# Optimization experiments

Measured on AMD Instinct MI355X. Metric: run time of the kernel, lower is better.

The kernel has to match this reference:

```python
import jax, jax.numpy as jnp
import numpy as np

N_NODES = 50000


def setup_inputs() -> dict:
    key = jax.random.key(0)
    k1, k2, k3, k4, k5, k6 = jax.random.split(key, 6)
    feature = jax.random.normal(k1, (N_NODES, 128), dtype=jnp.float32)
    norm = jax.random.uniform(k2, (N_NODES, 1), dtype=jnp.float32)
    W = jax.random.normal(k3, (128, 128), dtype=jnp.float32) * 0.05
    b = jax.random.normal(k4, (128,), dtype=jnp.float32) * 0.05
    src = jax.random.randint(k5, (600000,), 0, N_NODES, dtype=jnp.int32)
    dst = jax.random.randint(k6, (600000,), 0, N_NODES, dtype=jnp.int32)
    return {"feature": feature, "norm": norm, "W": W, "b": b, "src": src, "dst": dst}


def reference(feature, norm, W, b, src, dst):
    n = feature.shape[0]
    # message: h_src * norm_src, gathered per edge  [E, d]
    msg = feature[src] * norm[src]
    # scatter-sum into destination nodes, then scale by norm_dst
    accum = jax.ops.segment_sum(msg, dst, num_segments=n) * norm
    # DGL semantics: nodes with zero in-degree keep their original feature
    in_deg = jax.ops.segment_sum(jnp.ones((dst.shape[0],), dtype=jnp.float32), dst, num_segments=n)
    h = jnp.where(in_deg[:, None] > 0, accum, feature)
    # node apply: linear + relu
    return jax.nn.relu(h @ W.T + b)
```

## Files before the change

kernel.cpp:

```cpp
#include <hip/hip_runtime.h>

#define N_NODES 50000
#define N_EDGES 600000
#define D 128
#define CAP 64

typedef __attribute__((ext_vector_type(8))) short bf16x8;
typedef __attribute__((ext_vector_type(4))) float f32x4;
typedef __attribute__((ext_vector_type(4))) unsigned short ushort4v;

__device__ inline unsigned int f2bf_u(float f) {
    unsigned int u = __builtin_bit_cast(unsigned int, f);
    return (u + 0x7FFFu + ((u >> 16) & 1u)) >> 16;
}
__device__ inline unsigned int pack2(float lo, float hi) {
    return f2bf_u(lo) | (f2bf_u(hi) << 16);
}
__device__ inline float bf_lo(unsigned int u) {
    return __builtin_bit_cast(float, u << 16);
}
__device__ inline float bf_hi(unsigned int u) {
    return __builtin_bit_cast(float, u & 0xFFFF0000u);
}

__global__ __launch_bounds__(256) void setup_kernel(
    const float* __restrict__ W, unsigned short* __restrict__ Wb,
    int* __restrict__ cursor)
{
    const int b = blockIdx.x, t = threadIdx.x;
    if (b < 16) {
        int j = b * 256 + t;
        float4 w = *reinterpret_cast<const float4*>(W + (size_t)j * 4);
        ushort4 o;
        o.x = (unsigned short)f2bf_u(w.x);
        o.y = (unsigned short)f2bf_u(w.y);
        o.z = (unsigned short)f2bf_u(w.z);
        o.w = (unsigned short)f2bf_u(w.w);
        *reinterpret_cast<ushort4*>(Wb + (size_t)j * 4) = o;
    } else {
        int idx = (b - 16) * 256 + t;
        if (idx < 12500) *reinterpret_cast<int4*>(cursor + idx * 4) = make_int4(0, 0, 0, 0);
    }
}

__global__ __launch_bounds__(256) void prefill_kernel(
    const int* __restrict__ src, const int* __restrict__ dst,
    const float* __restrict__ feat, const float* __restrict__ norm,
    int* __restrict__ cursor, unsigned short* __restrict__ csr16,
    unsigned short* __restrict__ g)
{
    const int b = blockIdx.x, t = threadIdx.x;
    if (b < 2344) {
        int e = b * 256 + t;
        if (e < N_EDGES) {
            int d = dst[e];
            int slot = atomicAdd(&cursor[d], 1);
            if (slot < CAP) csr16[((size_t)d << 6) + slot] = (unsigned short)src[e];
        }
    } else {
        int gid = (b - 2344) * 256 + t;
        int row = gid >> 4;
        int c8  = (gid & 15) * 8;
        float nr = norm[row];
        float4 f0 = *reinterpret_cast<const float4*>(feat + (size_t)row * D + c8);
        float4 f1 = *reinterpret_cast<const float4*>(feat + (size_t)row * D + c8 + 4);
        uint4 o;
        o.x = pack2(f0.x * nr, f0.y * nr);
        o.y = pack2(f0.z * nr, f0.w * nr);
        o.z = pack2(f1.x * nr, f1.y * nr);
        o.w = pack2(f1.z * nr, f1.w * nr);
        *reinterpret_cast<uint4*>(g + (size_t)row * D + c8) = o;
    }
}

__global__ __launch_bounds__(256) void gather_mfma(
    const unsigned short* __restrict__ g,
    const float* __restrict__ feat, const float* __restrict__ norm,
    const int* __restrict__ cursor,
    const unsigned short* __restrict__ csr16,
    const unsigned short* __restrict__ Wb,
    const float* __restrict__ bias,
    float* __restrict__ out)
{
    __shared__ __align__(16) unsigned short hsh[16 * 136];
    const int t    = threadIdx.x;
    const int w    = t >> 6;
    const int lane = t & 63;
    const int kg   = lane >> 4;
    const int mr   = lane & 15;
    const int nbase = blockIdx.x * 16;

    const int ln   = w * 4 + kg;
    const int node = nbase + ln;
    const int deg  = min(cursor[node], CAP);
    const int base = node << 6;

    float a0 = 0.f, a1 = 0.f, a2 = 0.f, a3 = 0.f;
    float a4 = 0.f, a5 = 0.f, a6 = 0.f, a7 = 0.f;
    const unsigned short* gcol = g + mr * 8;

    int i = 0;
    for (; i + 4 <= deg; i += 4) {
        ushort4v ix = *reinterpret_cast<const ushort4v*>(csr16 + base + i);
        uint4 v0 = *reinterpret_cast<const uint4*>(gcol + (size_t)ix[0] * D);
        uint4 v1 = *reinterpret_cast<const uint4*>(gcol + (size_t)ix[1] * D);
        uint4 v2 = *reinterpret_cast<const uint4*>(gcol + (size_t)ix[2] * D);
        uint4 v3 = *reinterpret_cast<const uint4*>(gcol + (size_t)ix[3] * D);
        a0 += bf_lo(v0.x) + bf_lo(v1.x) + bf_lo(v2.x) + bf_lo(v3.x);
        a1 += bf_hi(v0.x) + bf_hi(v1.x) + bf_hi(v2.x) + bf_hi(v3.x);
        a2 += bf_lo(v0.y) + bf_lo(v1.y) + bf_lo(v2.y) + bf_lo(v3.y);
        a3 += bf_hi(v0.y) + bf_hi(v1.y) + bf_hi(v2.y) + bf_hi(v3.y);
        a4 += bf_lo(v0.z) + bf_lo(v1.z) + bf_lo(v2.z) + bf_lo(v3.z);
        a5 += bf_hi(v0.z) + bf_hi(v1.z) + bf_hi(v2.z) + bf_hi(v3.z);
        a6 += bf_lo(v0.w) + bf_lo(v1.w) + bf_lo(v2.w) + bf_lo(v3.w);
        a7 += bf_hi(v0.w) + bf_hi(v1.w) + bf_hi(v2.w) + bf_hi(v3.w);
    }
    for (; i < deg; ++i) {
        unsigned short s0 = csr16[base + i];
        uint4 v0 = *reinterpret_cast<const uint4*>(gcol + (size_t)s0 * D);
        a0 += bf_lo(v0.x); a1 += bf_hi(v0.x);
        a2 += bf_lo(v0.y); a3 += bf_hi(v0.y);
        a4 += bf_lo(v0.z); a5 += bf_hi(v0.z);
        a6 += bf_lo(v0.w); a7 += bf_hi(v0.w);
    }

    if (deg == 0) {
        float4 f0 = *reinterpret_cast<const float4*>(feat + (size_t)node * D + mr * 8);
        float4 f1 = *reinterpret_cast<const float4*>(feat + (size_t)node * D + mr * 8 + 4);
        a0 = f0.x; a1 = f0.y; a2 = f0.z; a3 = f0.w;
        a4 = f1.x; a5 = f1.y; a6 = f1.z; a7 = f1.w;
    } else {
        float nd = norm[node];
        a0 *= nd; a1 *= nd; a2 *= nd; a3 *= nd;
        a4 *= nd; a5 *= nd; a6 *= nd; a7 *= nd;
    }
    uint4 o;
    o.x = pack2(a0, a1);
    o.y = pack2(a2, a3);
    o.z = pack2(a4, a5);
    o.w = pack2(a6, a7);
    *reinterpret_cast<uint4*>(&hsh[ln * 136 + mr * 8]) = o;
    __syncthreads();

    bf16x8 fa0 = *reinterpret_cast<const bf16x8*>(&hsh[mr * 136 + kg * 8]);
    bf16x8 fa1 = *reinterpret_cast<const bf16x8*>(&hsh[mr * 136 + kg * 8 + 32]);
    bf16x8 fa2 = *reinterpret_cast<const bf16x8*>(&hsh[mr * 136 + kg * 8 + 64]);
    bf16x8 fa3 = *reinterpret_cast<const bf16x8*>(&hsh[mr * 136 + kg * 8 + 96]);

    const int orow0 = nbase + kg * 4;
    #pragma unroll
    for (int nn = 0; nn < 2; ++nn) {
        const int n0 = w * 2 + nn;
        const size_t bbase = (size_t)(n0 * 16 + mr) * D + kg * 8;
        bf16x8 b0 = *reinterpret_cast<const bf16x8*>(Wb + bbase);
        bf16x8 b1 = *reinterpret_cast<const bf16x8*>(Wb + bbase + 32);
        bf16x8 b2 = *reinterpret_cast<const bf16x8*>(Wb + bbase + 64);
        bf16x8 b3 = *reinterpret_cast<const bf16x8*>(Wb + bbase + 96);
        f32x4 acc = {0.f, 0.f, 0.f, 0.f};
        acc = __builtin_amdgcn_mfma_f32_16x16x32_bf16(fa0, b0, acc, 0, 0, 0);
        acc = __builtin_amdgcn_mfma_f32_16x16x32_bf16(fa1, b1, acc, 0, 0, 0);
        acc = __builtin_amdgcn_mfma_f32_16x16x32_bf16(fa2, b2, acc, 0, 0, 0);
        acc = __builtin_amdgcn_mfma_f32_16x16x32_bf16(fa3, b3, acc, 0, 0, 0);

        const int c = n0 * 16 + mr;
        const float bv = bias[c];
        #pragma unroll
        for (int j = 0; j < 4; ++j) {
            float r = acc[j] + bv;
            out[(size_t)(orow0 + j) * D + c] = r > 0.f ? r : 0.f;
        }
    }
}

extern "C" void kernel_launch(void* const* d_in, const int* in_sizes, int n_in,
                              void* d_out, int out_size, void* d_ws, size_t ws_size,
                              hipStream_t stream) {
    const float* feat = (const float*)d_in[0];
    const float* norm = (const float*)d_in[1];
    const float* W    = (const float*)d_in[2];
    const float* bias = (const float*)d_in[3];
    const int*   src  = (const int*)d_in[4];
    const int*   dst  = (const int*)d_in[5];
    float* out = (float*)d_out;

    char* ws = (char*)d_ws;
    unsigned short* g      = (unsigned short*)ws;
    int*            cursor = (int*)(ws + (size_t)N_NODES * D * sizeof(unsigned short));
    unsigned short* csr16  = (unsigned short*)(cursor + N_NODES);
    unsigned short* Wb     = csr16 + (size_t)N_NODES * CAP;

    setup_kernel<<<65, 256, 0, stream>>>(W, Wb, cursor);
    prefill_kernel<<<2344 + 3125, 256, 0, stream>>>(src, dst, feat, norm, cursor, csr16, g);
    gather_mfma<<<N_NODES / 16, 256, 0, stream>>>(g, feat, norm, cursor, csr16, Wb, bias, out);
}
```

Baseline: 83.72 us.

## Build edge buckets with per-chunk LDS histograms and prefix scan instead of global atomics

Replaces the global atomicAdd cursor bucketing with a deterministic three-stage build. Per-chunk shared-memory histograms are computed over destination quarters, a column-wise prefix scan across the 120 chunks gives each chunk its slot offsets and the node degrees, and a second pass fills the CSR using LDS atomics plus those offsets. The aim is to remove contended global atomics on the cursor array. In exchange it adds an extra kernel launch, large packed-16-bit histogram and prefix buffers in workspace, and a serial 120-step scan per thread. The W conversion and cursor zeroing move into the scan kernel.

```diff
diff --git a/kernel.cpp b/kernel.cpp
--- a/kernel.cpp
+++ b/kernel.cpp
@@ -4,6 +4,9 @@
 #define N_EDGES 600000
 #define D 128
 #define CAP 64
+#define C_CHUNKS 120
+#define CHUNK 5000
+#define QD 12500
 
 typedef __attribute__((ext_vector_type(8))) short bf16x8;
 typedef __attribute__((ext_vector_type(4))) float f32x4;
@@ -23,42 +26,51 @@
     return __builtin_bit_cast(float, u & 0xFFFF0000u);
 }
 
-__global__ __launch_bounds__(256) void setup_kernel(
-    const float* __restrict__ W, unsigned short* __restrict__ Wb,
-    int* __restrict__ cursor)
+__global__ __launch_bounds__(256) void hist_kernel(
+    const int* __restrict__ dst, unsigned int* __restrict__ hist_g)
+{
+    __shared__ unsigned int hist[QD];
+    const int c = blockIdx.x, t = threadIdx.x;
+    const int ebase = c * CHUNK;
+    for (int h = 0; h < 4; ++h) {
+        const int dlo = h * QD;
+        for (int j = t; j < QD; j += 256) hist[j] = 0;
+        __syncthreads();
+        for (int i = t; i < CHUNK; i += 256) {
+            int d = dst[ebase + i] - dlo;
+            if ((unsigned)d < (unsigned)QD) atomicAdd(&hist[d], 1u);
+        }
+        __syncthreads();
+        unsigned int* outp = hist_g + (size_t)c * 25000 + h * (QD / 2);
+        for (int p = t; p < QD / 2; p += 256)
+            outp[p] = (hist[2 * p] & 0xFFFFu) | (hist[2 * p + 1] << 16);
+        __syncthreads();
+    }
+}
+
+__global__ __launch_bounds__(256) void scanpre_kernel(
+    const unsigned int* __restrict__ hist_g, unsigned int* __restrict__ pfx_g,
+    int* __restrict__ deg,
+    const float* __restrict__ feat, const float* __restrict__ norm,
+    unsigned short* __restrict__ g,
+    const float* __restrict__ W, unsigned short* __restrict__ Wb)
 {
     const int b = blockIdx.x, t = threadIdx.x;
-    if (b < 16) {
-        int j = b * 256 + t;
-        float4 w = *reinterpret_cast<const float4*>(W + (size_t)j * 4);
-        ushort4 o;
-        o.x = (unsigned short)f2bf_u(w.x);
-        o.y = (unsigned short)f2bf_u(w.y);
-        o.z = (unsigned short)f2bf_u(w.z);
-        o.w = (unsigned short)f2bf_u(w.w);
-        *reinterpret_cast<ushort4*>(Wb + (size_t)j * 4) = o;
-    } else {
-        int idx = (b - 16) * 256 + t;
-        if (idx < 12500) *reinterpret_cast<int4*>(cursor + idx * 4) = make_int4(0, 0, 0, 0);
-    }
-}
-
-__global__ __launch_bounds__(256) void prefill_kernel(
-    const int* __restrict__ src, const int* __restrict__ dst,
-    const float* __restrict__ feat, const float* __restrict__ norm,
-    int* __restrict__ cursor, unsigned short* __restrict__ csr16,
-    unsigned short* __restrict__ g)
-{
-    const int b = blockIdx.x, t = threadIdx.x;
-    if (b < 2344) {
-        int e = b * 256 + t;
-        if (e < N_EDGES) {
-            int d = dst[e];
-            int slot = atomicAdd(&cursor[d], 1);
-            if (slot < CAP) csr16[((size_t)d << 6) + slot] = (unsigned short)src[e];
-        }
-    } else {
-        int gid = (b - 2344) * 256 + t;
+    if (b < 98) {
+        int q = b * 256 + t;
+        if (q < 25000) {
+            unsigned int r0 = 0, r1 = 0;
+            for (int c = 0; c < C_CHUNKS; ++c) {
+                unsigned int hv = hist_g[(size_t)c * 25000 + q];
+                pfx_g[(size_t)c * 25000 + q] = r0 | (r1 << 16);
+                r0 += hv & 0xFFFFu;
+                r1 += hv >> 16;
+            }
+            deg[2 * q]     = (int)r0;
+            deg[2 * q + 1] = (int)r1;
+        }
+    } else if (b < 98 + 3125) {
+        int gid = (b - 98) * 256 + t;
         int row = gid >> 4;
         int c8  = (gid & 15) * 8;
         float nr = norm[row];
@@ -70,13 +82,47 @@
         o.z = pack2(f1.x * nr, f1.y * nr);
         o.w = pack2(f1.z * nr, f1.w * nr);
         *reinterpret_cast<uint4*>(g + (size_t)row * D + c8) = o;
+    } else {
+        int j = (b - 98 - 3125) * 256 + t;
+        float4 w = *reinterpret_cast<const float4*>(W + (size_t)j * 4);
+        ushort4 o;
+        o.x = (unsigned short)f2bf_u(w.x);
+        o.y = (unsigned short)f2bf_u(w.y);
+        o.z = (unsigned short)f2bf_u(w.z);
+        o.w = (unsigned short)f2bf_u(w.w);
+        *reinterpret_cast<ushort4*>(Wb + (size_t)j * 4) = o;
+    }
+}
+
+__global__ __launch_bounds__(256) void fillc_kernel(
+    const int* __restrict__ src, const int* __restrict__ dst,
+    const unsigned int* __restrict__ pfx_g, unsigned short* __restrict__ csr16)
+{
+    __shared__ unsigned int hist[QD];
+    const int c = blockIdx.x, t = threadIdx.x;
+    const int ebase = c * CHUNK;
+    const unsigned short* pfx16 = (const unsigned short*)(pfx_g + (size_t)c * 25000);
+    for (int h = 0; h < 4; ++h) {
+        const int dlo = h * QD;
+        for (int j = t; j < QD; j += 256) hist[j] = 0;
+        __syncthreads();
+        for (int i = t; i < CHUNK; i += 256) {
+            int d = dst[ebase + i];
+            int dl = d - dlo;
+            if ((unsigned)dl < (unsigned)QD) {
+                unsigned int r = atomicAdd(&hist[dl], 1u);
+                unsigned int slot = (unsigned int)pfx16[d] + r;
+                if (slot < CAP) csr16[((size_t)d << 6) + slot] = (unsigned short)src[ebase + i];
+            }
+        }
+        __syncthreads();
     }
 }
 
 __global__ __launch_bounds__(256) void gather_mfma(
     const unsigned short* __restrict__ g,
     const float* __restrict__ feat, const float* __restrict__ norm,
-    const int* __restrict__ cursor,
+    const int* __restrict__ deg_arr,
     const unsigned short* __restrict__ csr16,
     const unsigned short* __restrict__ Wb,
     const float* __restrict__ bias,
@@ -92,7 +138,7 @@
 
     const int ln   = w * 4 + kg;
     const int node = nbase + ln;
-    const int deg  = min(cursor[node], CAP);
+    const int deg  = min(deg_arr[node], CAP);
     const int base = node << 6;
 
     float a0 = 0.f, a1 = 0.f, a2 = 0.f, a3 = 0.f;
@@ -185,11 +231,14 @@
 
     char* ws = (char*)d_ws;
     unsigned short* g      = (unsigned short*)ws;
-    int*            cursor = (int*)(ws + (size_t)N_NODES * D * sizeof(unsigned short));
-    unsigned short* csr16  = (unsigned short*)(cursor + N_NODES);
+    int*            deg    = (int*)(ws + (size_t)N_NODES * D * 2);
+    unsigned short* csr16  = (unsigned short*)(deg + N_NODES);
     unsigned short* Wb     = csr16 + (size_t)N_NODES * CAP;
-
-    setup_kernel<<<65, 256, 0, stream>>>(W, Wb, cursor);
-    prefill_kernel<<<2344 + 3125, 256, 0, stream>>>(src, dst, feat, norm, cursor, csr16, g);
-    gather_mfma<<<N_NODES / 16, 256, 0, stream>>>(g, feat, norm, cursor, csr16, Wb, bias, out);
-}
+    unsigned int*   hist_g = (unsigned int*)(Wb + 16384);
+    unsigned int*   pfx_g  = hist_g + (size_t)C_CHUNKS * 25000;
+
+    hist_kernel<<<C_CHUNKS, 256, 0, stream>>>(dst, hist_g);
+    scanpre_kernel<<<98 + 3125 + 16, 256, 0, stream>>>(hist_g, pfx_g, deg, feat, norm, g, W, Wb);
+    fillc_kernel<<<C_CHUNKS, 256, 0, stream>>>(src, dst, pfx_g, csr16);
+    gather_mfma<<<N_NODES / 16, 256, 0, stream>>>(g, feat, norm, deg, csr16, Wb, bias, out);
+}
```

New measurement: 132.6 us. 58.4% more time.

## Pad per-node atomic cursors to 64 bytes and fuse edge fill with premultiply threads

Applied to the files above, without the earlier changes.

Per-node degree counters now sit 16 ints (64 bytes) apart, so atomics on different destination nodes no longer share a cache line. The CSR fill and the feature premultiply-to-bf16 conversion now run in the same threads of one 3125-block grid instead of disjoint block ranges. This lets atomic latency overlap with the feature loads and stores. The cost is a 16x larger cursor array that must be zeroed each call, and scattered degree reads in the gather kernel.

```diff
diff --git a/kernel.cpp b/kernel.cpp
--- a/kernel.cpp
+++ b/kernel.cpp
@@ -4,6 +4,7 @@
 #define N_EDGES 600000
 #define D 128
 #define CAP 64
+#define CSTRIDE 16
 
 typedef __attribute__((ext_vector_type(8))) short bf16x8;
 typedef __attribute__((ext_vector_type(4))) float f32x4;
@@ -23,7 +24,7 @@
     return __builtin_bit_cast(float, u & 0xFFFF0000u);
 }
 
-__global__ __launch_bounds__(256) void setup_kernel(
+__global__ __launch_bounds__(256) void init_kernel(
     const float* __restrict__ W, unsigned short* __restrict__ Wb,
     int* __restrict__ cursor)
 {
@@ -39,26 +40,27 @@
         *reinterpret_cast<ushort4*>(Wb + (size_t)j * 4) = o;
     } else {
         int idx = (b - 16) * 256 + t;
-        if (idx < 12500) *reinterpret_cast<int4*>(cursor + idx * 4) = make_int4(0, 0, 0, 0);
+        if (idx < 200000) *reinterpret_cast<int4*>(cursor + idx * 4) = make_int4(0, 0, 0, 0);
     }
 }
 
-__global__ __launch_bounds__(256) void prefill_kernel(
+__global__ __launch_bounds__(256) void fill_premul(
     const int* __restrict__ src, const int* __restrict__ dst,
     const float* __restrict__ feat, const float* __restrict__ norm,
     int* __restrict__ cursor, unsigned short* __restrict__ csr16,
     unsigned short* __restrict__ g)
 {
-    const int b = blockIdx.x, t = threadIdx.x;
-    if (b < 2344) {
-        int e = b * 256 + t;
-        if (e < N_EDGES) {
-            int d = dst[e];
-            int slot = atomicAdd(&cursor[d], 1);
-            if (slot < CAP) csr16[((size_t)d << 6) + slot] = (unsigned short)src[e];
-        }
-    } else {
-        int gid = (b - 2344) * 256 + t;
+    const int gid = blockIdx.x * 256 + threadIdx.x;
+
+    int d = 0, sv = 0, slot = CAP;
+    const bool he = gid < N_EDGES;
+    if (he) {
+        d  = dst[gid];
+        sv = src[gid];
+        slot = atomicAdd(&cursor[d * CSTRIDE], 1);
+    }
+
+    {
         int row = gid >> 4;
         int c8  = (gid & 15) * 8;
         float nr = norm[row];
@@ -71,6 +73,8 @@
         o.w = pack2(f1.z * nr, f1.w * nr);
         *reinterpret_cast<uint4*>(g + (size_t)row * D + c8) = o;
     }
+
+    if (he && slot < CAP) csr16[((size_t)d << 6) + slot] = (unsigned short)sv;
 }
 
 __global__ __launch_bounds__(256) void gather_mfma(
@@ -92,7 +96,7 @@
 
     const int ln   = w * 4 + kg;
     const int node = nbase + ln;
-    const int deg  = min(cursor[node], CAP);
+    const int deg  = min(cursor[node * CSTRIDE], CAP);
     const int base = node << 6;
 
     float a0 = 0.f, a1 = 0.f, a2 = 0.f, a3 = 0.f;
@@ -185,11 +189,11 @@
 
     char* ws = (char*)d_ws;
     unsigned short* g      = (unsigned short*)ws;
-    int*            cursor = (int*)(ws + (size_t)N_NODES * D * sizeof(unsigned short));
-    unsigned short* csr16  = (unsigned short*)(cursor + N_NODES);
+    int*            cursor = (int*)(ws + (size_t)N_NODES * D * 2);
+    unsigned short* csr16  = (unsigned short*)(cursor + N_NODES * CSTRIDE);
     unsigned short* Wb     = csr16 + (size_t)N_NODES * CAP;
 
-    setup_kernel<<<65, 256, 0, stream>>>(W, Wb, cursor);
-    prefill_kernel<<<2344 + 3125, 256, 0, stream>>>(src, dst, feat, norm, cursor, csr16, g);
+    init_kernel<<<16 + 782, 256, 0, stream>>>(W, Wb, cursor);
+    fill_premul<<<3125, 256, 0, stream>>>(src, dst, feat, norm, cursor, csr16, g);
     gather_mfma<<<N_NODES / 16, 256, 0, stream>>>(g, feat, norm, cursor, csr16, Wb, bias, out);
 }
```

Result: faster. 80.86 us (-3.4%).
